# Performance work log

Hardware: AMD Instinct MI355X
Metric: run time of the kernel (lower is better)

The kernel has to match this reference:

```python
import jax, jax.numpy as jnp
import numpy as np

DIM = 2560
N_HEAD = 32
HEAD_DIM = 80
ROT_DIM = 32  # head_dim * partial_rotary_factor
INTER = 10240
EPS = 1e-5
BASE = 10000.0


def setup_inputs() -> dict:
    key = jax.random.key(0)
    ks = jax.random.split(key, 12)
    B, S, D, I = 1, 2048, DIM, INTER
    s = lambda k, shape, scale: (jax.random.normal(k, shape, jnp.float32) * scale)
    return {
        "x": s(ks[0], (B, S, D), 1.0),
        "input_pos": jnp.arange(S, dtype=jnp.int32),
        "mask": jnp.tril(jnp.ones((S, S), dtype=bool)),
        "ln_w": jnp.ones((D,), jnp.float32),
        "ln_b": jnp.zeros((D,), jnp.float32),
        "wqkv_w": s(ks[1], (3 * D, D), 0.02),
        "wqkv_b": jnp.zeros((3 * D,), jnp.float32),
        "wo_w": s(ks[2], (D, D), 0.02),
        "wo_b": jnp.zeros((D,), jnp.float32),
        "w1_w": s(ks[3], (I, D), 0.02),
        "w1_b": jnp.zeros((I,), jnp.float32),
        "w2_w": s(ks[4], (D, I), 0.02),
        "w2_b": jnp.zeros((D,), jnp.float32),
    }


def _rope_cos_sin(positions):
    # positions: [S] int; returns cos,sin of shape [S, ROT_DIM]
    inv_freq = 1.0 / (BASE ** (jnp.arange(0, ROT_DIM, 2, dtype=jnp.float32) / ROT_DIM))
    freqs = positions.astype(jnp.float32)[:, None] * inv_freq[None, :]  # [S, ROT/2]
    emb = jnp.concatenate([freqs, freqs], axis=-1)  # [S, ROT]
    return jnp.cos(emb), jnp.sin(emb)


def _rotate_half(t):
    t1, t2 = jnp.split(t, 2, axis=-1)
    return jnp.concatenate([-t2, t1], axis=-1)


def _apply_rope(t, cos, sin):
    # t: [B,H,S,hd]; rotary applied to first ROT_DIM dims (partial rotary)
    t_rot, t_pass = t[..., :ROT_DIM], t[..., ROT_DIM:]
    t_rot = t_rot * cos[None, None] + _rotate_half(t_rot) * sin[None, None]
    return jnp.concatenate([t_rot, t_pass], axis=-1)


def reference(x, input_pos, mask, ln_w, ln_b, wqkv_w, wqkv_b, wo_w, wo_b,
              w1_w, w1_b, w2_w, w2_b):
    B, S, D = x.shape
    H, hd = N_HEAD, HEAD_DIM
    # shared LayerNorm (parallel block)
    mu = jnp.mean(x, axis=-1, keepdims=True)
    var = jnp.mean(jnp.square(x - mu), axis=-1, keepdims=True)
    h = (x - mu) * jax.lax.rsqrt(var + EPS) * ln_w + ln_b

    # fused QKV
    qkv = h @ wqkv_w.T + wqkv_b  # [B,S,3D]
    q, k, v = jnp.split(qkv, 3, axis=-1)
    q = q.reshape(B, S, H, hd).transpose(0, 2, 1, 3)  # [B,H,S,hd]
    k = k.reshape(B, S, H, hd).transpose(0, 2, 1, 3)
    v = v.reshape(B, S, H, hd).transpose(0, 2, 1, 3)

    cos, sin = _rope_cos_sin(input_pos)
    q = _apply_rope(q, cos, sin)
    k = _apply_rope(k, cos, sin)

    # causal attention
    scores = jnp.einsum("bhqd,bhkd->bhqk", q, k) / np.sqrt(hd).astype(np.float32)
    scores = jnp.where(mask[None, None], scores, jnp.float32(-1e9))
    attn = jax.nn.softmax(scores, axis=-1)
    y = jnp.einsum("bhqk,bhkd->bhqd", attn, v)  # [B,H,S,hd]
    y = y.transpose(0, 2, 1, 3).reshape(B, S, D)
    attn_out = y @ wo_w.T + wo_b

    # fused MLP (phi2: gelu_new / tanh approx)
    ffn = jax.nn.gelu(h @ w1_w.T + w1_b, approximate=True) @ w2_w.T + w2_b

    return attn_out + ffn + x
```

## Files before the change

### kernel.cpp

```cpp
#include <hip/hip_runtime.h>
#include <cstdint>

#define S_LEN 2048
#define DMODEL 2560
#define NHEADS 32
#define HDIM 80
#define DINTER 10240

typedef unsigned short u16;
typedef __bf16 bf16x8 __attribute__((ext_vector_type(8)));
typedef float f32x4 __attribute__((ext_vector_type(4)));

__device__ __forceinline__ float us2f(u16 u) {
  return __builtin_bit_cast(float, ((uint32_t)u) << 16);
}
__device__ __forceinline__ u16 f2us(float f) {
  uint32_t x = __builtin_bit_cast(uint32_t, f);
  x += 0x7fffu + ((x >> 16) & 1u);
  return (u16)(x >> 16);
}

typedef __attribute__((address_space(1))) void gas_void;
typedef __attribute__((address_space(3))) void las_void;
__device__ __forceinline__ void gld16(const void* g, void* l) {
  __builtin_amdgcn_global_load_lds((gas_void*)g, (las_void*)l, 16, 0, 0);
}

__global__ void f2b_kernel(const float* __restrict__ src, u16* __restrict__ dst) {
  const size_t i = ((size_t)blockIdx.x * 256 + threadIdx.x) * 8;
  const float4 a = *(const float4*)(src + i);
  const float4 b = *(const float4*)(src + i + 4);
  u16 o[8] = {f2us(a.x), f2us(a.y), f2us(a.z), f2us(a.w),
              f2us(b.x), f2us(b.y), f2us(b.z), f2us(b.w)};
  *(uint4*)(dst + i) = *(uint4*)o;
}

__global__ void initout_kernel(const float* __restrict__ x,
                               const float* __restrict__ wo_b,
                               const float* __restrict__ w2_b,
                               float* __restrict__ out) {
  const size_t idx = ((size_t)blockIdx.x * 256 + threadIdx.x) * 4;
  const int c0 = (int)(idx % DMODEL);
  const float4 vx = *(const float4*)(x + idx);
  const float4 b1 = *(const float4*)(wo_b + c0);
  const float4 b2 = *(const float4*)(w2_b + c0);
  float4 vo;
  vo.x = vx.x + b1.x + b2.x;
  vo.y = vx.y + b1.y + b2.y;
  vo.z = vx.z + b1.z + b2.z;
  vo.w = vx.w + b1.w + b2.w;
  *(float4*)(out + idx) = vo;
}

__global__ void ln_kernel(const float* __restrict__ x, const float* __restrict__ w,
                          const float* __restrict__ b, u16* __restrict__ h) {
  const int s = blockIdx.x, tid = threadIdx.x;
  const float* xr = x + (size_t)s * DMODEL;
  float v[10];
  float sum = 0.f, sq = 0.f;
#pragma unroll
  for (int j = 0; j < 10; j++) {
    v[j] = xr[tid + j * 256];
    sum += v[j];
    sq += v[j] * v[j];
  }
#pragma unroll
  for (int o = 32; o > 0; o >>= 1) {
    sum += __shfl_down(sum, o, 64);
    sq += __shfl_down(sq, o, 64);
  }
  __shared__ float red[8];
  const int wave = tid >> 6, lane = tid & 63;
  if (lane == 0) { red[wave] = sum; red[4 + wave] = sq; }
  __syncthreads();
  sum = red[0] + red[1] + red[2] + red[3];
  sq = red[4] + red[5] + red[6] + red[7];
  const float mu = sum * (1.0f / DMODEL);
  const float var = sq * (1.0f / DMODEL) - mu * mu;
  const float rstd = rsqrtf(var + 1e-5f);
  u16* hr = h + (size_t)s * DMODEL;
#pragma unroll
  for (int j = 0; j < 10; j++) {
    const int d = tid + j * 256;
    hr[d] = f2us((v[j] - mu) * rstd * w[d] + b[d]);
  }
}

template <int ACT, int MODE>
__global__ void gemm_bt(const u16* __restrict__ A, const u16* __restrict__ B,
                        const float* __restrict__ bias, void* __restrict__ Cv,
                        int M, int N, int K) {
  __shared__ __align__(16) u16 As[128 * 32];
  __shared__ __align__(16) u16 Bs[128 * 32];
  const int tid = threadIdx.x;
  const int wave = tid >> 6, lane = tid & 63;
  const int quad = lane >> 4, l15 = lane & 15;
  const int wm = wave >> 1, wn = wave & 1;

  const int flat = blockIdx.x + gridDim.x * blockIdx.y;
  const int r_ = flat & 63;
  const int bn = (flat >> 6) * 4 + (r_ & 3);
  const int bm = r_ >> 2;

  const int Kc = K / gridDim.z;
  const int kbeg = blockIdx.z * Kc;

  const int srow = lane >> 2;
  const int scol = (((lane & 3) ^ ((lane >> 4) & 3)) * 8);
  const size_t aBase = (size_t)(bm * 128 + wave * 32 + srow) * K + scol;
  const size_t aBase2 = aBase + (size_t)16 * K;
  const size_t bBase = (size_t)(bn * 128 + wave * 32 + srow) * K + scol;
  const size_t bBase2 = bBase + (size_t)16 * K;
  u16* AsW0 = As + (wave * 32) * 32;
  u16* AsW1 = As + (wave * 32 + 16) * 32;
  u16* BsW0 = Bs + (wave * 32) * 32;
  u16* BsW1 = Bs + (wave * 32 + 16) * 32;

  const int fcol = (quad ^ ((l15 >> 2) & 3)) * 8;

  f32x4 acc[4][4] = {};

  for (int k0 = kbeg; k0 < kbeg + Kc; k0 += 32) {
    gld16(A + aBase + k0, AsW0);
    gld16(A + aBase2 + k0, AsW1);
    gld16(B + bBase + k0, BsW0);
    gld16(B + bBase2 + k0, BsW1);
    __syncthreads();
    bf16x8 af[4], bf[4];
#pragma unroll
    for (int mt = 0; mt < 4; mt++)
      af[mt] = *(const bf16x8*)&As[(wm * 64 + mt * 16 + l15) * 32 + fcol];
#pragma unroll
    for (int nt = 0; nt < 4; nt++)
      bf[nt] = *(const bf16x8*)&Bs[(wn * 64 + nt * 16 + l15) * 32 + fcol];
#pragma unroll
    for (int mt = 0; mt < 4; mt++)
#pragma unroll
      for (int nt = 0; nt < 4; nt++)
        acc[mt][nt] =
            __builtin_amdgcn_mfma_f32_16x16x32_bf16(af[mt], bf[nt], acc[mt][nt], 0, 0, 0);
    __syncthreads();
  }

#pragma unroll
  for (int nt = 0; nt < 4; nt++) {
    const int col = bn * 128 + wn * 64 + nt * 16 + l15;
    const float bv = (MODE == 0) ? bias[col] : 0.f;
#pragma unroll
    for (int mt = 0; mt < 4; mt++) {
      const int row0 = bm * 128 + wm * 64 + mt * 16 + quad * 4;
#pragma unroll
      for (int r = 0; r < 4; r++) {
        float v = acc[mt][nt][r] + bv;
        if (ACT == 1) {
          const float t = v * (0.7978845608f + 0.0356774081f * v * v);
          v = 0.5f * v * (1.0f + tanhf(t));
        }
        if (MODE == 0)
          ((u16*)Cv)[(size_t)(row0 + r) * N + col] = f2us(v);
        else
          atomicAdd((float*)Cv + (size_t)(row0 + r) * N + col, v);
      }
    }
  }
}

__global__ void rope_kernel(u16* __restrict__ qkv, const int* __restrict__ pos) {
  const int idx = blockIdx.x * 256 + threadIdx.x;
  const int i = idx & 15;
  const int which = (idx >> 4) & 1;
  const int hh = (idx >> 5) & 31;
  const int s = idx >> 10;
  const float p = (float)pos[s];
  const float freq = p * expf(-0.57564627324851f * (float)i);
  float sn, c;
  sincosf(freq, &sn, &c);
  u16* base = qkv + (size_t)s * (3 * DMODEL) + which * DMODEL + hh * HDIM + i;
  const float t0 = us2f(base[0]), t1 = us2f(base[16]);
  base[0] = f2us(t0 * c - t1 * sn);
  base[16] = f2us(t1 * c + t0 * sn);
}

__global__ void attn_kernel(const u16* __restrict__ qkv, u16* __restrict__ y) {
  const int qt = (int)gridDim.x - 1 - (int)blockIdx.x;
  const int h = blockIdx.y;
  const int tid = threadIdx.x, wave = tid >> 6, lane = tid & 63;
  const int quad = lane >> 4, l15 = lane & 15;
  const int qbase = qt * 64;

  __shared__ __align__(16) u16 Qs[64 * 104];
  __shared__ __align__(16) u16 Ks[64 * 104];
  __shared__ __align__(16) u16 Vts[80 * 88];
  __shared__ __align__(16) u16 Ps[4][2][16 * 40];

  for (int i = tid; i < 64 * 104; i += 256) { Qs[i] = 0; Ks[i] = 0; }
  __syncthreads();

  {
    const int r = tid >> 2, c = tid & 3;
    const u16* src = qkv + (size_t)(qbase + r) * (3 * DMODEL) + h * HDIM + c * 20;
    u16* dst = Qs + r * 104 + c * 20;
#pragma unroll
    for (int j = 0; j < 5; j++) {
      ushort4 uv = *(const ushort4*)(src + j * 4);
      ushort4 ov;
      ov.x = f2us(us2f(uv.x) * 0.11180339887f);
      ov.y = f2us(us2f(uv.y) * 0.11180339887f);
      ov.z = f2us(us2f(uv.z) * 0.11180339887f);
      ov.w = f2us(us2f(uv.w) * 0.11180339887f);
      *(ushort4*)(dst + j * 4) = ov;
    }
  }

  float m_i[4], l_i[4];
  f32x4 oacc[5] = {};
#pragma unroll
  for (int r = 0; r < 4; r++) { m_i[r] = -1e30f; l_i[r] = 0.f; }

  const int n_iter = qt + 1;
  __syncthreads();

  for (int it = 0; it < n_iter; ++it) {
    const int kc0 = it * 64;
    if (tid < 128) {
      const int r = tid >> 1, c = (tid & 1) * 40;
      const u16* src =
          qkv + (size_t)(kc0 + r) * (3 * DMODEL) + DMODEL + h * HDIM + c;
      u16* dst = Ks + r * 104 + c;
#pragma unroll
      for (int j = 0; j < 10; j++)
        *(ushort4*)(dst + j * 4) = *(const ushort4*)(src + j * 4);
    } else {
      const int u = tid - 128;
      const int r = u >> 1, c0 = (u & 1) * 40;
      const u16* src =
          qkv + (size_t)(kc0 + r) * (3 * DMODEL) + 2 * DMODEL + h * HDIM + c0;
#pragma unroll
      for (int j = 0; j < 10; j++) {
        ushort4 vv = *(const ushort4*)(src + j * 4);
        const int d0 = c0 + j * 4;
        Vts[(d0 + 0) * 88 + r] = vv.x;
        Vts[(d0 + 1) * 88 + r] = vv.y;
        Vts[(d0 + 2) * 88 + r] = vv.z;
        Vts[(d0 + 3) * 88 + r] = vv.w;
      }
    }
    __syncthreads();

    f32x4 st[4] = {};
    bf16x8 aq[3];
#pragma unroll
    for (int ks = 0; ks < 3; ks++)
      aq[ks] = *(const bf16x8*)&Qs[(wave * 16 + l15) * 104 + ks * 32 + quad * 8];
#pragma unroll
    for (int ks = 0; ks < 3; ks++)
#pragma unroll
      for (int t = 0; t < 4; t++) {
        bf16x8 bk = *(const bf16x8*)&Ks[(t * 16 + l15) * 104 + ks * 32 + quad * 8];
        st[t] = __builtin_amdgcn_mfma_f32_16x16x32_bf16(aq[ks], bk, st[t], 0, 0, 0);
      }

    float sv[4][4], mx[4];
#pragma unroll
    for (int r = 0; r < 4; r++) {
      const int qr = qbase + wave * 16 + quad * 4 + r;
#pragma unroll
      for (int t = 0; t < 4; t++) {
        const int kc = kc0 + t * 16 + l15;
        sv[t][r] = (kc <= qr) ? st[t][r] : -1e30f;
      }
      mx[r] = fmaxf(fmaxf(sv[0][r], sv[1][r]), fmaxf(sv[2][r], sv[3][r]));
    }
#pragma unroll
    for (int o = 1; o < 16; o <<= 1)
#pragma unroll
      for (int r = 0; r < 4; r++) mx[r] = fmaxf(mx[r], __shfl_xor(mx[r], o, 64));

    float alpha[4], rs[4];
#pragma unroll
    for (int r = 0; r < 4; r++) {
      const float mnew = fmaxf(m_i[r], mx[r]);
      alpha[r] = __expf(m_i[r] - mnew);
      m_i[r] = mnew;
      const float p0 = __expf(sv[0][r] - mnew);
      const float p1 = __expf(sv[1][r] - mnew);
      const float p2 = __expf(sv[2][r] - mnew);
      const float p3 = __expf(sv[3][r] - mnew);
      rs[r] = (p0 + p1) + (p2 + p3);
      const int ro = (quad * 4 + r) * 40;
      Ps[wave][0][ro + l15] = f2us(p0);
      Ps[wave][0][ro + 16 + l15] = f2us(p1);
      Ps[wave][1][ro + l15] = f2us(p2);
      Ps[wave][1][ro + 16 + l15] = f2us(p3);
    }
#pragma unroll
    for (int o = 1; o < 16; o <<= 1)
#pragma unroll
      for (int r = 0; r < 4; r++) rs[r] += __shfl_xor(rs[r], o, 64);
#pragma unroll
    for (int r = 0; r < 4; r++) l_i[r] = l_i[r] * alpha[r] + rs[r];
#pragma unroll
    for (int dt = 0; dt < 5; dt++)
#pragma unroll
      for (int r = 0; r < 4; r++) oacc[dt][r] *= alpha[r];

    bf16x8 pf0 = *(const bf16x8*)&Ps[wave][0][l15 * 40 + quad * 8];
    bf16x8 pf1 = *(const bf16x8*)&Ps[wave][1][l15 * 40 + quad * 8];
#pragma unroll
    for (int dt = 0; dt < 5; dt++) {
      bf16x8 vf0 = *(const bf16x8*)&Vts[(dt * 16 + l15) * 88 + quad * 8];
      bf16x8 vf1 = *(const bf16x8*)&Vts[(dt * 16 + l15) * 88 + 32 + quad * 8];
      oacc[dt] = __builtin_amdgcn_mfma_f32_16x16x32_bf16(pf0, vf0, oacc[dt], 0, 0, 0);
      oacc[dt] = __builtin_amdgcn_mfma_f32_16x16x32_bf16(pf1, vf1, oacc[dt], 0, 0, 0);
    }
    __syncthreads();
  }

#pragma unroll
  for (int dt = 0; dt < 5; dt++)
#pragma unroll
    for (int r = 0; r < 4; r++) {
      const int row = qbase + wave * 16 + quad * 4 + r;
      y[(size_t)row * DMODEL + h * HDIM + dt * 16 + l15] = f2us(oacc[dt][r] / l_i[r]);
    }
}

extern "C" void kernel_launch(void* const* d_in, const int* in_sizes, int n_in,
                              void* d_out, int out_size, void* d_ws, size_t ws_size,
                              hipStream_t stream) {
  const float* x = (const float*)d_in[0];
  const int* pos = (const int*)d_in[1];
  const float* ln_w = (const float*)d_in[3];
  const float* ln_b = (const float*)d_in[4];
  const float* wqkv_w = (const float*)d_in[5];
  const float* wqkv_b = (const float*)d_in[6];
  const float* wo_w = (const float*)d_in[7];
  const float* wo_b = (const float*)d_in[8];
  const float* w1_w = (const float*)d_in[9];
  const float* w1_b = (const float*)d_in[10];
  const float* w2_w = (const float*)d_in[11];
  const float* w2_b = (const float*)d_in[12];
  float* out = (float*)d_out;

  char* ws = (char*)d_ws;
  u16* wbuf = (u16*)(ws);
  u16* h = (u16*)(ws + 52428800);
  u16* ffn1 = (u16*)(ws + 62914560);
  u16* qkv = (u16*)(ws + 62914560);
  u16* yAtt = (u16*)(ws + 94371840);

  ln_kernel<<<S_LEN, 256, 0, stream>>>(x, ln_w, ln_b, h);
  initout_kernel<<<(S_LEN * DMODEL / 4) / 256, 256, 0, stream>>>(x, wo_b, w2_b, out);

  f2b_kernel<<<(DINTER * DMODEL) / 2048, 256, 0, stream>>>(w1_w, wbuf);
  gemm_bt<1, 0><<<dim3(DINTER / 128, S_LEN / 128, 1), 256, 0, stream>>>(
      h, wbuf, w1_b, ffn1, S_LEN, DINTER, DMODEL);
  f2b_kernel<<<(DMODEL * DINTER) / 2048, 256, 0, stream>>>(w2_w, wbuf);
  gemm_bt<0, 2><<<dim3(DMODEL / 128, S_LEN / 128, 4), 256, 0, stream>>>(
      ffn1, wbuf, w2_b, out, S_LEN, DMODEL, DINTER);

  f2b_kernel<<<(3 * DMODEL * DMODEL) / 2048, 256, 0, stream>>>(wqkv_w, wbuf);
  gemm_bt<0, 0><<<dim3(3 * DMODEL / 128, S_LEN / 128, 1), 256, 0, stream>>>(
      h, wbuf, wqkv_b, qkv, S_LEN, 3 * DMODEL, DMODEL);
  rope_kernel<<<(S_LEN * NHEADS * 2 * 16) / 256, 256, 0, stream>>>(qkv, pos);
  attn_kernel<<<dim3(S_LEN / 64, NHEADS), 256, 0, stream>>>(qkv, yAtt);
  f2b_kernel<<<(DMODEL * DMODEL) / 2048, 256, 0, stream>>>(wo_w, wbuf);
  gemm_bt<0, 2><<<dim3(DMODEL / 128, S_LEN / 128, 2), 256, 0, stream>>>(
      yAtt, wbuf, wo_b, out, S_LEN, DMODEL, DMODEL);
}
```

Baseline: 1.005 ms.

## Replace 128x128 GEMM with double-buffered 256x256 tile, 8-wave pipelined kernel

Replaces the single-buffered 128x128 tile GEMM with a 256x256 tile kernel using 512 threads, BK=64 and double-buffered LDS. Global-to-LDS loads for the next k-step are interleaved with MFMA quadrants using explicit vmcnt waits and barriers, and MFMA sections raise wave priority. It also adds an XCD-aware block swizzle and changes the split-K for the w2 GEMM from 4 to 5. The aim is to raise data reuse per tile and hide load latency behind compute, at the cost of fewer workgroups, a larger LDS footprint and fragile hand-tuned wait counts.

```diff
diff --git a/kernel.cpp b/kernel.cpp
--- a/kernel.cpp
+++ b/kernel.cpp
@@ -25,6 +25,14 @@
 __device__ __forceinline__ void gld16(const void* g, void* l) {
   __builtin_amdgcn_global_load_lds((gas_void*)g, (las_void*)l, 16, 0, 0);
 }
+
+#define VMW(N) asm volatile("s_waitcnt vmcnt(" #N ")" ::: "memory")
+#define BARRIER()                          \
+  do {                                     \
+    asm volatile("" ::: "memory");         \
+    __builtin_amdgcn_s_barrier();          \
+    asm volatile("" ::: "memory");         \
+  } while (0)
 
 __global__ void f2b_kernel(const float* __restrict__ src, u16* __restrict__ dst) {
   const size_t i = ((size_t)blockIdx.x * 256 + threadIdx.x) * 8;
@@ -87,82 +95,177 @@
 }
 
 template <int ACT, int MODE>
-__global__ void gemm_bt(const u16* __restrict__ A, const u16* __restrict__ B,
+__launch_bounds__(512, 2)
+__global__ void gemm256(const u16* __restrict__ A, const u16* __restrict__ B,
                         const float* __restrict__ bias, void* __restrict__ Cv,
                         int M, int N, int K) {
-  __shared__ __align__(16) u16 As[128 * 32];
-  __shared__ __align__(16) u16 Bs[128 * 32];
+  __shared__ __align__(16) u16 lds[4][16384];
   const int tid = threadIdx.x;
-  const int wave = tid >> 6, lane = tid & 63;
+  const int w = tid >> 6, lane = tid & 63;
   const int quad = lane >> 4, l15 = lane & 15;
-  const int wm = wave >> 1, wn = wave & 1;
-
+  const int wm = w >> 2, wn = w & 3;
+
+  const int nwg = gridDim.x * gridDim.y;
   const int flat = blockIdx.x + gridDim.x * blockIdx.y;
-  const int r_ = flat & 63;
-  const int bn = (flat >> 6) * 4 + (r_ & 3);
-  const int bm = r_ >> 2;
+  const int swz = (flat & 7) * (nwg >> 3) + (flat >> 3);
+  const int ntN = N >> 8;
+  const int bm = swz / ntN, bn = swz % ntN;
 
   const int Kc = K / gridDim.z;
-  const int kbeg = blockIdx.z * Kc;
-
-  const int srow = lane >> 2;
-  const int scol = (((lane & 3) ^ ((lane >> 4) & 3)) * 8);
-  const size_t aBase = (size_t)(bm * 128 + wave * 32 + srow) * K + scol;
-  const size_t aBase2 = aBase + (size_t)16 * K;
-  const size_t bBase = (size_t)(bn * 128 + wave * 32 + srow) * K + scol;
-  const size_t bBase2 = bBase + (size_t)16 * K;
-  u16* AsW0 = As + (wave * 32) * 32;
-  u16* AsW1 = As + (wave * 32 + 16) * 32;
-  u16* BsW0 = Bs + (wave * 32) * 32;
-  u16* BsW1 = Bs + (wave * 32 + 16) * 32;
-
-  const int fcol = (quad ^ ((l15 >> 2) & 3)) * 8;
-
-  f32x4 acc[4][4] = {};
-
-  for (int k0 = kbeg; k0 < kbeg + Kc; k0 += 32) {
-    gld16(A + aBase + k0, AsW0);
-    gld16(A + aBase2 + k0, AsW1);
-    gld16(B + bBase + k0, BsW0);
-    gld16(B + bBase2 + k0, BsW1);
-    __syncthreads();
-    bf16x8 af[4], bf[4];
-#pragma unroll
-    for (int mt = 0; mt < 4; mt++)
-      af[mt] = *(const bf16x8*)&As[(wm * 64 + mt * 16 + l15) * 32 + fcol];
-#pragma unroll
-    for (int nt = 0; nt < 4; nt++)
-      bf[nt] = *(const bf16x8*)&Bs[(wn * 64 + nt * 16 + l15) * 32 + fcol];
-#pragma unroll
-    for (int mt = 0; mt < 4; mt++)
-#pragma unroll
-      for (int nt = 0; nt < 4; nt++)
-        acc[mt][nt] =
-            __builtin_amdgcn_mfma_f32_16x16x32_bf16(af[mt], bf[nt], acc[mt][nt], 0, 0, 0);
-    __syncthreads();
-  }
-
-#pragma unroll
-  for (int nt = 0; nt < 4; nt++) {
-    const int col = bn * 128 + wn * 64 + nt * 16 + l15;
-    const float bv = (MODE == 0) ? bias[col] : 0.f;
-#pragma unroll
-    for (int mt = 0; mt < 4; mt++) {
-      const int row0 = bm * 128 + wm * 64 + mt * 16 + quad * 4;
-#pragma unroll
-      for (int r = 0; r < 4; r++) {
-        float v = acc[mt][nt][r] + bv;
-        if (ACT == 1) {
-          const float t = v * (0.7978845608f + 0.0356774081f * v * v);
-          v = 0.5f * v * (1.0f + tanhf(t));
+  const int k0 = blockIdx.z * Kc;
+  const int nk = Kc >> 6;
+
+  const int stgCol = ((lane & 7) * 8) ^ (((lane >> 5) & 1) * 16);
+  const u16* Ag = A + ((size_t)bm * 256 + w * 8 + (lane >> 3)) * K + k0 + stgCol;
+  const u16* Bg = B + ((size_t)bn * 256 + w * 8 + (lane >> 3)) * K + k0 + stgCol;
+
+  const int qa = (quad * 8) ^ (((l15 >> 2) & 1) * 16);
+  const int arow = wm * 64 + l15;
+  const int brow = wn * 32 + l15;
+
+#define STG_HALF(MAT, GP, BUF, HF, KT)                                       \
+  do {                                                                       \
+    gld16((GP) + (size_t)((HF) * 128) * K + (KT) * 64,                       \
+          &lds[(BUF) * 2 + (MAT)][(HF) * 8192 + w * 512]);                   \
+    gld16((GP) + (size_t)((HF) * 128 + 64) * K + (KT) * 64,                  \
+          &lds[(BUF) * 2 + (MAT)][(HF) * 8192 + 4096 + w * 512]);            \
+  } while (0)
+
+#define LD_A(BUF, MH)                                                        \
+  _Pragma("unroll") for (int mf_ = 0; mf_ < 4; mf_++)                        \
+  _Pragma("unroll") for (int kk_ = 0; kk_ < 2; kk_++)                        \
+      aF[mf_][kk_] = *(const bf16x8*)&lds[(BUF) * 2]                         \
+          [(arow + (MH) * 128 + mf_ * 16) * 64 + kk_ * 32 + qa];
+
+#define LD_B(DST, BUF, NH)                                                   \
+  _Pragma("unroll") for (int nf_ = 0; nf_ < 2; nf_++)                        \
+  _Pragma("unroll") for (int kk_ = 0; kk_ < 2; kk_++)                        \
+      DST[nf_][kk_] = *(const bf16x8*)&lds[(BUF) * 2 + 1]                    \
+          [(brow + (NH) * 128 + nf_ * 16) * 64 + kk_ * 32 + qa];
+
+#define MFMA_Q(MH, NH, BF)                                                   \
+  do {                                                                       \
+    __builtin_amdgcn_s_setprio(1);                                           \
+    _Pragma("unroll") for (int kk_ = 0; kk_ < 2; kk_++)                      \
+    _Pragma("unroll") for (int mf_ = 0; mf_ < 4; mf_++)                      \
+    _Pragma("unroll") for (int nf_ = 0; nf_ < 2; nf_++)                      \
+        acc[(MH) * 4 + mf_][(NH) * 2 + nf_] =                                \
+            __builtin_amdgcn_mfma_f32_16x16x32_bf16(                         \
+                aF[mf_][kk_], BF[nf_][kk_],                                  \
+                acc[(MH) * 4 + mf_][(NH) * 2 + nf_], 0, 0, 0);               \
+    __builtin_amdgcn_s_setprio(0);                                           \
+  } while (0)
+
+  f32x4 acc[8][4] = {};
+  bf16x8 aF[4][2], bF0[2][2], bF1[2][2];
+
+  STG_HALF(0, Ag, 0, 0, 0);
+  STG_HALF(1, Bg, 0, 0, 0);
+  STG_HALF(1, Bg, 0, 1, 0);
+  STG_HALF(0, Ag, 0, 1, 0);
+  STG_HALF(0, Ag, 1, 0, 1);
+  VMW(6);
+  BARRIER();
+
+  for (int t = 0; t < nk - 2; ++t) {
+    const int bc = t & 1, ob = bc ^ 1;
+    LD_A(bc, 0);
+    LD_B(bF0, bc, 0);
+    STG_HALF(1, Bg, ob, 0, t + 1);
+    VMW(6);
+    BARRIER();
+    MFMA_Q(0, 0, bF0);
+    BARRIER();
+    LD_B(bF1, bc, 1);
+    STG_HALF(1, Bg, ob, 1, t + 1);
+    VMW(6);
+    BARRIER();
+    MFMA_Q(0, 1, bF1);
+    BARRIER();
+    LD_A(bc, 1);
+    STG_HALF(0, Ag, ob, 1, t + 1);
+    BARRIER();
+    MFMA_Q(1, 1, bF1);
+    BARRIER();
+    STG_HALF(0, Ag, bc, 0, t + 2);
+    VMW(6);
+    BARRIER();
+    MFMA_Q(1, 0, bF0);
+    BARRIER();
+  }
+  {
+    const int bc = (nk - 2) & 1, ob = bc ^ 1;
+    LD_A(bc, 0);
+    LD_B(bF0, bc, 0);
+    STG_HALF(1, Bg, ob, 0, nk - 1);
+    VMW(6);
+    BARRIER();
+    MFMA_Q(0, 0, bF0);
+    BARRIER();
+    LD_B(bF1, bc, 1);
+    STG_HALF(1, Bg, ob, 1, nk - 1);
+    VMW(6);
+    BARRIER();
+    MFMA_Q(0, 1, bF1);
+    BARRIER();
+    LD_A(bc, 1);
+    STG_HALF(0, Ag, ob, 1, nk - 1);
+    BARRIER();
+    MFMA_Q(1, 1, bF1);
+    BARRIER();
+    VMW(4);
+    BARRIER();
+    MFMA_Q(1, 0, bF0);
+    BARRIER();
+  }
+  {
+    const int bc = (nk - 1) & 1;
+    LD_A(bc, 0);
+    LD_B(bF0, bc, 0);
+    VMW(2);
+    BARRIER();
+    MFMA_Q(0, 0, bF0);
+    BARRIER();
+    LD_B(bF1, bc, 1);
+    VMW(0);
+    BARRIER();
+    MFMA_Q(0, 1, bF1);
+    BARRIER();
+    LD_A(bc, 1);
+    BARRIER();
+    MFMA_Q(1, 1, bF1);
+    MFMA_Q(1, 0, bF0);
+  }
+
+#pragma unroll
+  for (int nh = 0; nh < 2; nh++)
+#pragma unroll
+    for (int nf = 0; nf < 2; nf++) {
+      const int col = bn * 256 + nh * 128 + wn * 32 + nf * 16 + l15;
+      const float bv = (MODE == 0) ? bias[col] : 0.f;
+#pragma unroll
+      for (int mh = 0; mh < 2; mh++)
+#pragma unroll
+        for (int mf = 0; mf < 4; mf++) {
+          const int row0 = bm * 256 + mh * 128 + wm * 64 + mf * 16 + quad * 4;
+#pragma unroll
+          for (int r = 0; r < 4; r++) {
+            float v = acc[mh * 4 + mf][nh * 2 + nf][r] + bv;
+            if (ACT == 1) {
+              const float tt = v * (0.7978845608f + 0.0356774081f * v * v);
+              v = 0.5f * v * (1.0f + tanhf(tt));
+            }
+            if (MODE == 0)
+              ((u16*)Cv)[(size_t)(row0 + r) * N + col] = f2us(v);
+            else
+              atomicAdd((float*)Cv + (size_t)(row0 + r) * N + col, v);
+          }
         }
-        if (MODE == 0)
-          ((u16*)Cv)[(size_t)(row0 + r) * N + col] = f2us(v);
-        else
-          atomicAdd((float*)Cv + (size_t)(row0 + r) * N + col, v);
-      }
-    }
-  }
+    }
+#undef STG_HALF
+#undef LD_A
+#undef LD_B
+#undef MFMA_Q
 }
 
 __global__ void rope_kernel(u16* __restrict__ qkv, const int* __restrict__ pos) {
@@ -353,18 +456,18 @@
   initout_kernel<<<(S_LEN * DMODEL / 4) / 256, 256, 0, stream>>>(x, wo_b, w2_b, out);
 
   f2b_kernel<<<(DINTER * DMODEL) / 2048, 256, 0, stream>>>(w1_w, wbuf);
-  gemm_bt<1, 0><<<dim3(DINTER / 128, S_LEN / 128, 1), 256, 0, stream>>>(
+  gemm256<1, 0><<<dim3(DINTER / 256, S_LEN / 256, 1), 512, 0, stream>>>(
       h, wbuf, w1_b, ffn1, S_LEN, DINTER, DMODEL);
   f2b_kernel<<<(DMODEL * DINTER) / 2048, 256, 0, stream>>>(w2_w, wbuf);
-  gemm_bt<0, 2><<<dim3(DMODEL / 128, S_LEN / 128, 4), 256, 0, stream>>>(
+  gemm256<0, 2><<<dim3(DMODEL / 256, S_LEN / 256, 5), 512, 0, stream>>>(
       ffn1, wbuf, w2_b, out, S_LEN, DMODEL, DINTER);
 
   f2b_kernel<<<(3 * DMODEL * DMODEL) / 2048, 256, 0, stream>>>(wqkv_w, wbuf);
-  gemm_bt<0, 0><<<dim3(3 * DMODEL / 128, S_LEN / 128, 1), 256, 0, stream>>>(
+  gemm256<0, 0><<<dim3(3 * DMODEL / 256, S_LEN / 256, 1), 512, 0, stream>>>(
       h, wbuf, wqkv_b, qkv, S_LEN, 3 * DMODEL, DMODEL);
   rope_kernel<<<(S_LEN * NHEADS * 2 * 16) / 256, 256, 0, stream>>>(qkv, pos);
   attn_kernel<<<dim3(S_LEN / 64, NHEADS), 256, 0, stream>>>(qkv, yAtt);
   f2b_kernel<<<(DMODEL * DMODEL) / 2048, 256, 0, stream>>>(wo_w, wbuf);
-  gemm_bt<0, 2><<<dim3(DMODEL / 128, S_LEN / 128, 2), 256, 0, stream>>>(
+  gemm256<0, 2><<<dim3(DMODEL / 256, S_LEN / 256, 2), 512, 0, stream>>>(
       yAtt, wbuf, wo_b, out, S_LEN, DMODEL, DMODEL);
 }
```

Result: no change. 1.009 ms (+0.4%).

## Replace GEMM with 256x256-tile, 512-thread, 4-stage pipelined LDS kernel

Applied to the files above, without the earlier changes.

Replaces the 128x128 single-buffered GEMM with a 256x256 tile kernel using 8 waves and a 4-deep LDS ring filled by async global-to-LDS loads. Explicit vmcnt waits and raw barriers let loads for tile k+3 and LDS fragment reads overlap the MFMA work, and s_setprio raises priority around the MFMA blocks. A new workgroup swizzle and a different split-K count for the w2 GEMM go with it. The larger tiles increase register and LDS pressure, and the lower block count may reduce occupancy for the small wo GEMM.

```diff
diff --git a/kernel.cpp b/kernel.cpp
--- a/kernel.cpp
+++ b/kernel.cpp
@@ -25,6 +25,14 @@
 __device__ __forceinline__ void gld16(const void* g, void* l) {
   __builtin_amdgcn_global_load_lds((gas_void*)g, (las_void*)l, 16, 0, 0);
 }
+
+#define VMW(N) asm volatile("s_waitcnt vmcnt(" #N ")" ::: "memory")
+#define BARRIER()                          \
+  do {                                     \
+    asm volatile("" ::: "memory");         \
+    __builtin_amdgcn_s_barrier();          \
+    asm volatile("" ::: "memory");         \
+  } while (0)
 
 __global__ void f2b_kernel(const float* __restrict__ src, u16* __restrict__ dst) {
   const size_t i = ((size_t)blockIdx.x * 256 + threadIdx.x) * 8;
@@ -87,82 +95,122 @@
 }
 
 template <int ACT, int MODE>
-__global__ void gemm_bt(const u16* __restrict__ A, const u16* __restrict__ B,
+__launch_bounds__(512, 2)
+__global__ void gemm256(const u16* __restrict__ A, const u16* __restrict__ B,
                         const float* __restrict__ bias, void* __restrict__ Cv,
                         int M, int N, int K) {
-  __shared__ __align__(16) u16 As[128 * 32];
-  __shared__ __align__(16) u16 Bs[128 * 32];
+  __shared__ __align__(16) u16 lds[4][16384];
   const int tid = threadIdx.x;
-  const int wave = tid >> 6, lane = tid & 63;
+  const int w = tid >> 6, lane = tid & 63;
   const int quad = lane >> 4, l15 = lane & 15;
-  const int wm = wave >> 1, wn = wave & 1;
-
+  const int wm = w >> 2, wn = w & 3;
+
+  const int nwg = gridDim.x * gridDim.y;
   const int flat = blockIdx.x + gridDim.x * blockIdx.y;
-  const int r_ = flat & 63;
-  const int bn = (flat >> 6) * 4 + (r_ & 3);
-  const int bm = r_ >> 2;
+  const int swz = (flat & 7) * (nwg >> 3) + (flat >> 3);
+  const int ntN = N >> 8;
+  const int bm = swz / ntN, bn = swz % ntN;
 
   const int Kc = K / gridDim.z;
-  const int kbeg = blockIdx.z * Kc;
-
-  const int srow = lane >> 2;
-  const int scol = (((lane & 3) ^ ((lane >> 4) & 3)) * 8);
-  const size_t aBase = (size_t)(bm * 128 + wave * 32 + srow) * K + scol;
-  const size_t aBase2 = aBase + (size_t)16 * K;
-  const size_t bBase = (size_t)(bn * 128 + wave * 32 + srow) * K + scol;
-  const size_t bBase2 = bBase + (size_t)16 * K;
-  u16* AsW0 = As + (wave * 32) * 32;
-  u16* AsW1 = As + (wave * 32 + 16) * 32;
-  u16* BsW0 = Bs + (wave * 32) * 32;
-  u16* BsW1 = Bs + (wave * 32 + 16) * 32;
-
-  const int fcol = (quad ^ ((l15 >> 2) & 3)) * 8;
-
-  f32x4 acc[4][4] = {};
-
-  for (int k0 = kbeg; k0 < kbeg + Kc; k0 += 32) {
-    gld16(A + aBase + k0, AsW0);
-    gld16(A + aBase2 + k0, AsW1);
-    gld16(B + bBase + k0, BsW0);
-    gld16(B + bBase2 + k0, BsW1);
-    __syncthreads();
-    bf16x8 af[4], bf[4];
-#pragma unroll
-    for (int mt = 0; mt < 4; mt++)
-      af[mt] = *(const bf16x8*)&As[(wm * 64 + mt * 16 + l15) * 32 + fcol];
-#pragma unroll
-    for (int nt = 0; nt < 4; nt++)
-      bf[nt] = *(const bf16x8*)&Bs[(wn * 64 + nt * 16 + l15) * 32 + fcol];
-#pragma unroll
-    for (int mt = 0; mt < 4; mt++)
-#pragma unroll
-      for (int nt = 0; nt < 4; nt++)
-        acc[mt][nt] =
-            __builtin_amdgcn_mfma_f32_16x16x32_bf16(af[mt], bf[nt], acc[mt][nt], 0, 0, 0);
-    __syncthreads();
-  }
-
-#pragma unroll
-  for (int nt = 0; nt < 4; nt++) {
-    const int col = bn * 128 + wn * 64 + nt * 16 + l15;
+  const int k0 = Kc * blockIdx.z;
+  const int nt = Kc >> 5;
+
+  const size_t k128 = (size_t)128 * K;
+  const u16* Ag = A + ((size_t)(bm * 256 + (tid >> 2))) * K + k0 + (tid & 3) * 8;
+  const u16* Bg = B + ((size_t)(bn * 256 + (tid >> 2))) * K + k0 + (tid & 3) * 8;
+  const int wDst = w * 512;
+
+  const int aRd = (wm * 128 + l15) * 32 + quad * 8;
+  const int bRd = 8192 + (wn * 64 + l15) * 32 + quad * 8;
+
+#define STAGE(W)                                                             \
+  do {                                                                       \
+    const int q_ = (W) & 3;                                                  \
+    const size_t ko_ = (size_t)(W) * 32;                                     \
+    gld16(Ag + ko_, &lds[q_][wDst]);                                         \
+    gld16(Ag + k128 + ko_, &lds[q_][4096 + wDst]);                           \
+    gld16(Bg + ko_, &lds[q_][8192 + wDst]);                                  \
+    gld16(Bg + k128 + ko_, &lds[q_][12288 + wDst]);                          \
+  } while (0)
+
+#define LD_A(DST, QB, PH)                                                    \
+  _Pragma("unroll") for (int mf_ = 0; mf_ < 4; mf_++)                        \
+      DST[mf_] = *(const bf16x8*)&lds[QB][aRd + (PH) * 2048 + mf_ * 512];
+
+#define LD_B(DST, QB)                                                        \
+  _Pragma("unroll") for (int nf_ = 0; nf_ < 4; nf_++)                        \
+      DST[nf_] = *(const bf16x8*)&lds[QB][bRd + nf_ * 512];
+
+#define MFMA_HALF(PH, AF, BF)                                                \
+  do {                                                                       \
+    __builtin_amdgcn_s_setprio(1);                                           \
+    _Pragma("unroll") for (int mf_ = 0; mf_ < 4; mf_++)                      \
+    _Pragma("unroll") for (int nf_ = 0; nf_ < 4; nf_++)                      \
+        acc[(PH) * 4 + mf_][nf_] = __builtin_amdgcn_mfma_f32_16x16x32_bf16(  \
+            AF[mf_], BF[nf_], acc[(PH) * 4 + mf_][nf_], 0, 0, 0);            \
+    __builtin_amdgcn_s_setprio(0);                                           \
+  } while (0)
+
+#define TILE(U, BCUR, BNXT)                                                  \
+  do {                                                                       \
+    const int q_ = (U) & 3;                                                  \
+    LD_A(aP1, q_, 1);                                                        \
+    MFMA_HALF(0, aP0, BCUR);                                                 \
+    if ((U) + 2 < nt) { VMW(4); } else { VMW(0); }                           \
+    BARRIER();                                                               \
+    if ((U) + 3 < nt) STAGE((U) + 3);                                        \
+    if ((U) + 1 < nt) {                                                      \
+      const int qn_ = ((U) + 1) & 3;                                         \
+      LD_A(aP0, qn_, 0);                                                     \
+      LD_B(BNXT, qn_);                                                       \
+    }                                                                        \
+    MFMA_HALF(1, aP1, BCUR);                                                 \
+  } while (0)
+
+  f32x4 acc[8][4] = {};
+  bf16x8 aP0[4], aP1[4], bE[4], bO[4];
+
+  STAGE(0);
+  STAGE(1);
+  STAGE(2);
+  VMW(8);
+  BARRIER();
+  LD_A(aP0, 0, 0);
+  LD_B(bE, 0);
+
+  for (int u = 0; u < nt; u += 2) {
+    TILE(u, bE, bO);
+    TILE(u + 1, bO, bE);
+  }
+
+#pragma unroll
+  for (int nf = 0; nf < 4; nf++) {
+    const int col = bn * 256 + wn * 64 + nf * 16 + l15;
     const float bv = (MODE == 0) ? bias[col] : 0.f;
 #pragma unroll
-    for (int mt = 0; mt < 4; mt++) {
-      const int row0 = bm * 128 + wm * 64 + mt * 16 + quad * 4;
-#pragma unroll
-      for (int r = 0; r < 4; r++) {
-        float v = acc[mt][nt][r] + bv;
-        if (ACT == 1) {
-          const float t = v * (0.7978845608f + 0.0356774081f * v * v);
-          v = 0.5f * v * (1.0f + tanhf(t));
+    for (int ph = 0; ph < 2; ph++)
+#pragma unroll
+      for (int mf = 0; mf < 4; mf++) {
+        const int row0 = bm * 256 + wm * 128 + ph * 64 + mf * 16 + quad * 4;
+#pragma unroll
+        for (int r = 0; r < 4; r++) {
+          float v = acc[ph * 4 + mf][nf][r] + bv;
+          if (ACT == 1) {
+            const float tt = v * (0.7978845608f + 0.0356774081f * v * v);
+            v = 0.5f * v * (1.0f + tanhf(tt));
+          }
+          if (MODE == 0)
+            ((u16*)Cv)[(size_t)(row0 + r) * N + col] = f2us(v);
+          else
+            atomicAdd((float*)Cv + (size_t)(row0 + r) * N + col, v);
         }
-        if (MODE == 0)
-          ((u16*)Cv)[(size_t)(row0 + r) * N + col] = f2us(v);
-        else
-          atomicAdd((float*)Cv + (size_t)(row0 + r) * N + col, v);
       }
-    }
-  }
+  }
+#undef STAGE
+#undef LD_A
+#undef LD_B
+#undef MFMA_HALF
+#undef TILE
 }
 
 __global__ void rope_kernel(u16* __restrict__ qkv, const int* __restrict__ pos) {
@@ -353,18 +401,18 @@
   initout_kernel<<<(S_LEN * DMODEL / 4) / 256, 256, 0, stream>>>(x, wo_b, w2_b, out);
 
   f2b_kernel<<<(DINTER * DMODEL) / 2048, 256, 0, stream>>>(w1_w, wbuf);
-  gemm_bt<1, 0><<<dim3(DINTER / 128, S_LEN / 128, 1), 256, 0, stream>>>(
+  gemm256<1, 0><<<dim3(DINTER / 256, S_LEN / 256, 1), 512, 0, stream>>>(
       h, wbuf, w1_b, ffn1, S_LEN, DINTER, DMODEL);
   f2b_kernel<<<(DMODEL * DINTER) / 2048, 256, 0, stream>>>(w2_w, wbuf);
-  gemm_bt<0, 2><<<dim3(DMODEL / 128, S_LEN / 128, 4), 256, 0, stream>>>(
+  gemm256<0, 2><<<dim3(DMODEL / 256, S_LEN / 256, 5), 512, 0, stream>>>(
       ffn1, wbuf, w2_b, out, S_LEN, DMODEL, DINTER);
 
   f2b_kernel<<<(3 * DMODEL * DMODEL) / 2048, 256, 0, stream>>>(wqkv_w, wbuf);
-  gemm_bt<0, 0><<<dim3(3 * DMODEL / 128, S_LEN / 128, 1), 256, 0, stream>>>(
+  gemm256<0, 0><<<dim3(3 * DMODEL / 256, S_LEN / 256, 1), 512, 0, stream>>>(
       h, wbuf, wqkv_b, qkv, S_LEN, 3 * DMODEL, DMODEL);
   rope_kernel<<<(S_LEN * NHEADS * 2 * 16) / 256, 256, 0, stream>>>(qkv, pos);
   attn_kernel<<<dim3(S_LEN / 64, NHEADS), 256, 0, stream>>>(qkv, yAtt);
   f2b_kernel<<<(DMODEL * DMODEL) / 2048, 256, 0, stream>>>(wo_w, wbuf);
-  gemm_bt<0, 2><<<dim3(DMODEL / 128, S_LEN / 128, 2), 256, 0, stream>>>(
+  gemm256<0, 2><<<dim3(DMODEL / 256, S_LEN / 256, 2), 512, 0, stream>>>(
       yAtt, wbuf, wo_b, out, S_LEN, DMODEL, DMODEL);
 }
```

New measurement: 1.028 ms. 2.3% more time.
